# Optimization experiments

Measured on AMD Instinct MI355X. Metric: run time of the kernel, lower is better.

## Reference

```python
import jax, jax.numpy as jnp
import numpy as np
from jax import lax

B, C, N, T, K = 16, 64, 512, 64, 3
EPS = 1e-5


def _bn(x, g, b):
    # training-mode BatchNorm2d over (B, H=N, W=T) per channel
    m = jnp.mean(x, axis=(0, 2, 3), keepdims=True)
    v = jnp.var(x, axis=(0, 2, 3), keepdims=True)
    return (x - m) * lax.rsqrt(v + EPS) * g[None, :, None, None] + b[None, :, None, None]


def _conv(x, w, b, pad):
    y = lax.conv_general_dilated(x, w, (1, 1), ((0, 0), pad),
                                 dimension_numbers=('NCHW', 'OIHW', 'NCHW'))
    return y + b[None, :, None, None]


def setup_inputs() -> dict:
    key = jax.random.key(0)
    ks = jax.random.split(key, 8)
    xav = lambda k, sh, fi, fo: jax.random.normal(k, sh, jnp.float32) * np.sqrt(2.0 / (fi + fo))
    return {
        'x': jax.random.normal(ks[0], (B, C, N, T), jnp.float32),
        'adj_mx': jax.random.normal(ks[1], (K, N, N), jnp.float32) / np.sqrt(N),
        'cheb_w': xav(ks[2], (K, C, C), C, C),
        'cheb_b': jnp.zeros((C,), jnp.float32),
        'w1': xav(ks[3], (C, C, 1, 3), 3 * C, 3 * C),
        'b1': jnp.zeros((C,), jnp.float32),
        'g1': jnp.ones((C,), jnp.float32),
        'be1': jnp.zeros((C,), jnp.float32),
        'w2': xav(ks[4], (C, C, 1, 3), 3 * C, 3 * C),
        'b2': jnp.zeros((C,), jnp.float32),
        'g2': jnp.ones((C,), jnp.float32),
        'be2': jnp.zeros((C,), jnp.float32),
        'gate_w': xav(ks[5], (C, 2 * C, 1, 1), 2 * C, C),
        'gate_b': jnp.zeros((C,), jnp.float32),
        'res_w': xav(ks[6], (C, C, 1, 1), C, C),
        'res_b': jnp.zeros((C,), jnp.float32),
        'g3': jnp.ones((C,), jnp.float32),
        'be3': jnp.zeros((C,), jnp.float32),
    }


def _forward(x, adj_mx, cheb_w, cheb_b, w1, b1, g1, be1, w2, b2, g2, be2,
             gate_w, gate_b, res_w, res_b, g3, be3):
    # ChebFilterBlock: out[b,o,n,t] = sum_{k,i,m} x[b,i,m,t] adj[k,m,n] W[k,i,o] + bias
    spatial = jnp.einsum('bimt,kmn,kio->bont', x, adj_mx, cheb_w) \
              + cheb_b[None, :, None, None]
    # temporal branch: two (1,3) convs with BN+ReLU
    t = jax.nn.relu(_bn(_conv(x, w1, b1, (1, 1)), g1, be1))
    t = jax.nn.relu(_bn(_conv(t, w2, b2, (1, 1)), g2, be2))
    # gated fusion
    comb = jnp.concatenate([spatial, t], axis=1)
    gate = jax.nn.sigmoid(_conv(comb, gate_w, gate_b, (0, 0)))
    res = _conv(x, res_w, res_b, (0, 0))
    out = gate * spatial + (1.0 - gate) * t + res
    return _bn(out, g3, be3)


def reference(x, adj_mx, cheb_w, cheb_b, w1, b1, g1, be1, w2, b2, g2, be2,
              gate_w, gate_b, res_w, res_b, g3, be3):
    return _forward(x, adj_mx, cheb_w, cheb_b, w1, b1, g1, be1, w2, b2, g2, be2,
                    gate_w, gate_b, res_w, res_b, g3, be3)
```

## Files before the change

kernel.cpp:

```cpp
#include <hip/hip_runtime.h>
#include <hip/hip_bf16.h>
#include <cstdint>

#define BB 16
#define CC 64
#define NN 512
#define TT 64
#define KCH 3
#define PP (BB*NN*TT)
#define EPSB 1e-5f

typedef __bf16 bf16;
typedef __bf16 bf16x8 __attribute__((ext_vector_type(8)));
typedef __bf16 bf16x4 __attribute__((ext_vector_type(4)));
typedef float  f32x4  __attribute__((ext_vector_type(4)));

#define MFMA16(A,Bv,Cv) __builtin_amdgcn_mfma_f32_16x16x32_bf16((A),(Bv),(Cv),0,0,0)

__device__ __forceinline__ void gload_lds16(const bf16* g, bf16* l){
  __builtin_amdgcn_global_load_lds(
      (const __attribute__((address_space(1))) void*)g,
      (__attribute__((address_space(3))) void*)l, 16, 0, 0);
}

__global__ __launch_bounds__(256) void k_adjT(const float* __restrict__ adj,
                                              bf16* __restrict__ adjb){
  int idx = blockIdx.x*256 + threadIdx.x;
  int m = idx & 511, n = (idx >> 9) & 511, k = idx >> 18;
  adjb[idx] = (bf16)adj[((size_t)(k*512 + m))*512 + n];
}

__global__ __launch_bounds__(256) void k_wprep(const float* __restrict__ w1,
    const float* __restrict__ w2, const float* __restrict__ cw,
    const float* __restrict__ gw, const float* __restrict__ rw,
    bf16* __restrict__ w1p, bf16* __restrict__ w2p, bf16* __restrict__ cp,
    bf16* __restrict__ gp, bf16* __restrict__ rp){
  int tid = threadIdx.x;
  for (int e = tid; e < 6*2048; e += 256){
    int j = e&7, lane = (e>>3)&63, cf = (e>>9)&3, ks = e>>11;
    int k = ks*32 + (lane>>4)*8 + j, col = cf*16 + (lane&15);
    int kk = k >> 6, i = k & 63;
    w1p[e] = (bf16)w1[(col*64 + i)*3 + kk];
    w2p[e] = (bf16)w2[(col*64 + i)*3 + kk];
    cp[e]  = (bf16)cw[((size_t)kk*64 + i)*64 + col];
  }
  for (int e = tid; e < 4*2048; e += 256){
    int j = e&7, lane = (e>>3)&63, cf = (e>>9)&3, ks = e>>11;
    int k = ks*32 + (lane>>4)*8 + j, col = cf*16 + (lane&15);
    gp[e] = (bf16)gw[col*128 + k];
  }
  for (int e = tid; e < 2*2048; e += 256){
    int j = e&7, lane = (e>>3)&63, cf = (e>>9)&3, ks = e>>11;
    int k = ks*32 + (lane>>4)*8 + j, col = cf*16 + (lane&15);
    rp[e] = (bf16)rw[col*64 + k];
  }
}

__global__ __launch_bounds__(256) void k_xlb(const float* __restrict__ x,
                                             bf16* __restrict__ xlb){
  __shared__ float tile[64][65];
  int bn = blockIdx.x; int b = bn >> 9, n = bn & 511;
  int tid = threadIdx.x;
  const float* xp = x + ((size_t)(b*64)*512 + n)*64;
  for (int p = 0; p < 4; ++p){
    int q = p*256 + tid;
    int i = q >> 4, tc = (q & 15)*4;
    float4 v = *reinterpret_cast<const float4*>(xp + (size_t)i*512*64 + tc);
    tile[i][tc+0] = v.x; tile[i][tc+1] = v.y; tile[i][tc+2] = v.z; tile[i][tc+3] = v.w;
  }
  __syncthreads();
  bf16* op = xlb + (size_t)bn*4096;
  for (int p = 0; p < 2; ++p){
    int v8 = p*256 + tid;
    int t = v8 >> 3, ic = (v8 & 7)*8;
    bf16x8 o;
    #pragma unroll
    for (int e = 0; e < 8; ++e) o[e] = (bf16)tile[ic+e][t];
    *reinterpret_cast<bf16x8*>(op + t*64 + ic) = o;
  }
}

__global__ __launch_bounds__(256) void k_xmt(const float* __restrict__ x,
                                             bf16* __restrict__ xmt){
  __shared__ bf16 T[32768];
  int bid = blockIdx.x;
  int b = bid >> 6, i0 = ((bid >> 3) & 7)*8, m0 = (bid & 7)*64;
  int tid = threadIdx.x;
  #pragma unroll 4
  for (int it = 0; it < 32; ++it){
    int flat = it*256 + tid;
    int t4 = flat & 15, m = (flat >> 4) & 63, i = flat >> 10;
    float4 v = *reinterpret_cast<const float4*>(
        x + ((size_t)((b*64 + i0 + i)*512) + (m0 + m))*64 + t4*4);
    int im = i*64 + m;
    int slot = t4 ^ ((m ^ i) & 15);
    bf16x4 pk; pk[0] = (bf16)v.x; pk[1] = (bf16)v.y; pk[2] = (bf16)v.z; pk[3] = (bf16)v.w;
    *reinterpret_cast<bf16x4*>(&T[im*64 + slot*4]) = pk;
  }
  __syncthreads();
  #pragma unroll 4
  for (int it = 0; it < 16; ++it){
    int flat = it*256 + tid;
    int mc = flat & 7, i = (flat >> 3) & 7, t = flat >> 6;
    bf16x8 o;
    #pragma unroll
    for (int e = 0; e < 8; ++e){
      int m = mc*8 + e;
      int slot = (t >> 2) ^ ((m ^ i) & 15);
      o[e] = T[(i*64 + m)*64 + slot*4 + (t & 3)];
    }
    *reinterpret_cast<bf16x8*>(
        &xmt[((size_t)((b*64 + t)*64) + i0 + i)*512 + m0 + mc*8]) = o;
  }
}

__global__ __launch_bounds__(256,4) void k_conv(const bf16* __restrict__ in,
    const bf16* __restrict__ wp, bf16* __restrict__ outp, float* __restrict__ part,
    const float* __restrict__ sc, const float* __restrict__ sh){
  int tid = threadIdx.x, w = tid >> 6, l = tid & 63, l15 = l & 15, lg = l >> 4;
  int blk = blockIdx.x;
  size_t rowbase = (size_t)blk * 64;
  const bf16* xr = in + rowbase * 64;
  int t = w*16 + l15;
  f32x4 acc[4] = {};
  #pragma unroll
  for (int ks = 0; ks < 6; ++ks){
    int dt = ks >> 1, kh = ks & 1;
    int ts = t + dt - 1;
    bf16x8 a = {};
    if (ts >= 0 && ts < 64){
      a = *reinterpret_cast<const bf16x8*>(xr + ts*64 + kh*32 + lg*8);
      if (sc){
        int i0 = kh*32 + lg*8;
        #pragma unroll
        for (int e = 0; e < 8; ++e){
          float f = (float)a[e]*sc[i0+e] + sh[i0+e];
          a[e] = (bf16)fmaxf(f, 0.f);
        }
      }
    }
    #pragma unroll
    for (int cf = 0; cf < 4; ++cf){
      bf16x8 bfr = *reinterpret_cast<const bf16x8*>(wp + ((ks*4 + cf)*64 + l)*8);
      acc[cf] = MFMA16(a, bfr, acc[cf]);
    }
  }
  __shared__ float ssum[4][4][16], ssq[4][4][16];
  #pragma unroll
  for (int cf = 0; cf < 4; ++cf){
    int o = cf*16 + l15;
    float s = 0.f, q = 0.f;
    #pragma unroll
    for (int r = 0; r < 4; ++r){
      float vv = acc[cf][r];
      int to = w*16 + lg*4 + r;
      outp[(rowbase + to)*64 + o] = (bf16)vv;
      s += vv; q += vv*vv;
    }
    s += __shfl_xor(s, 16); s += __shfl_xor(s, 32);
    q += __shfl_xor(q, 16); q += __shfl_xor(q, 32);
    if (lg == 0){ ssum[w][cf][l15] = s; ssq[w][cf][l15] = q; }
  }
  __syncthreads();
  if (tid < 64){
    int cf = tid >> 4, c = tid & 15;
    float s = ssum[0][cf][c]+ssum[1][cf][c]+ssum[2][cf][c]+ssum[3][cf][c];
    float q = ssq[0][cf][c]+ssq[1][cf][c]+ssq[2][cf][c]+ssq[3][cf][c];
    part[(size_t)blk*128 + tid*2]     = s;
    part[(size_t)blk*128 + tid*2 + 1] = q;
  }
}

__global__ __launch_bounds__(256) void k_stats(const float* __restrict__ part, int nb,
    const float* __restrict__ g, const float* __restrict__ be,
    float* __restrict__ sc, float* __restrict__ sh){
  int c = blockIdx.x, tid = threadIdx.x;
  float s = 0.f, q = 0.f;
  for (int i = tid; i < nb; i += 256){
    s += part[(size_t)i*128 + c*2];
    q += part[(size_t)i*128 + c*2 + 1];
  }
  __shared__ float rs[256], rq[256];
  rs[tid] = s; rq[tid] = q; __syncthreads();
  for (int st = 128; st > 0; st >>= 1){
    if (tid < st){ rs[tid] += rs[tid+st]; rq[tid] += rq[tid+st]; }
    __syncthreads();
  }
  if (tid == 0){
    float cnt = (float)PP;
    float mean = rs[0]/cnt, var = rq[0]/cnt - mean*mean;
    float r = rsqrtf(var + EPSB);
    sc[c] = g[c]*r;
    sh[c] = be[c] - mean*g[c]*r;
  }
}

__global__ __launch_bounds__(256,3) void k_gemm1(const bf16* __restrict__ xmt,
    const bf16* __restrict__ adjb, const bf16* __restrict__ cp,
    const float* __restrict__ cb, bf16* __restrict__ spm){
  __shared__ bf16 As[2][4096];
  __shared__ bf16 Bs[2][4096];
  __shared__ bf16 VT[64*128];

  int tid = threadIdx.x, w = tid >> 6, l = tid & 63, l15 = l & 15, lg = l >> 4;
  int wr = w >> 1, wc = w & 1;

  int orig = blockIdx.x;
  int wg = (orig & 7) * 256 + (orig >> 3);
  int jt = wg >> 2, nt = wg & 3;
  int J0 = jt*128, N0 = nt*128;

  const bf16* aglob = xmt + (size_t)J0*512;
  const bf16* bbase = adjb + (size_t)N0*512;

  auto stage = [&](int t){
    int buf = t & 1;
    const bf16* bg = bbase + (size_t)(t >> 4)*512*512;
    int m0 = (t & 15)*32;
    #pragma unroll
    for (int p = 0; p < 2; ++p){
      int idx = p*256 + tid;
      int r = idx >> 2, c = idx & 3;
      int cg = c ^ (r & 3);
      gload_lds16(aglob + (size_t)r*512 + m0 + cg*8,
                  &As[buf][(p*256 + w*64)*8]);
      gload_lds16(bg + (size_t)r*512 + m0 + cg*8,
                  &Bs[buf][(p*256 + w*64)*8]);
    }
  };

  f32x4 acc[4][4] = {};
  f32x4 acc2[4][4] = {};

  stage(0);
  for (int t = 0; t < 48; ++t){
    if (t < 47){
      stage(t+1);
      asm volatile("s_waitcnt vmcnt(4)" ::: "memory");
    } else {
      asm volatile("s_waitcnt vmcnt(0)" ::: "memory");
    }
    __builtin_amdgcn_s_barrier();
    __builtin_amdgcn_sched_barrier(0);

    int buf = t & 1;
    bf16x8 a[4], bb[4];
    #pragma unroll
    for (int rf = 0; rf < 4; ++rf){
      int row = wr*64 + rf*16 + l15;
      a[rf] = *reinterpret_cast<const bf16x8*>(
          &As[buf][row*32 + ((lg ^ (row & 3))*8)]);
    }
    #pragma unroll
    for (int cf = 0; cf < 4; ++cf){
      int row = wc*64 + cf*16 + l15;
      bb[cf] = *reinterpret_cast<const bf16x8*>(
          &Bs[buf][row*32 + ((lg ^ (row & 3))*8)]);
    }
    #pragma unroll
    for (int rf = 0; rf < 4; ++rf)
      #pragma unroll
      for (int cf = 0; cf < 4; ++cf)
        acc[rf][cf] = MFMA16(a[rf], bb[cf], acc[rf][cf]);

    asm volatile("s_waitcnt lgkmcnt(0)" ::: "memory");
    __builtin_amdgcn_sched_barrier(0);
    __builtin_amdgcn_s_barrier();

    if ((t & 15) == 15){
      int kk = t >> 4;
      #pragma unroll
      for (int h = 0; h < 2; ++h){
        if (wc == h){
          #pragma unroll
          for (int rf = 0; rf < 4; ++rf){
            int jb = wr*8 + rf*2 + (lg >> 1);
            #pragma unroll
            for (int cf = 0; cf < 4; ++cf){
              int nh = cf*16 + l15;
              bf16x4 pk;
              #pragma unroll
              for (int r = 0; r < 4; ++r) pk[r] = (bf16)acc[rf][cf][r];
              *reinterpret_cast<bf16x4*>(
                  &VT[nh*128 + ((jb ^ (nh & 15)) << 3) + ((lg & 1) << 2)]) = pk;
            }
          }
        }
        asm volatile("s_waitcnt lgkmcnt(0)" ::: "memory");
        __builtin_amdgcn_sched_barrier(0);
        __builtin_amdgcn_s_barrier();

        #pragma unroll
        for (int ks2 = 0; ks2 < 2; ++ks2){
          bf16x8 bc[4];
          #pragma unroll
          for (int cf = 0; cf < 4; ++cf)
            bc[cf] = *reinterpret_cast<const bf16x8*>(
                cp + (((kk*2 + ks2)*4 + cf)*64 + l)*8);
          #pragma unroll
          for (int rf2 = 0; rf2 < 2; ++rf2){
            int nh = (w & 1)*32 + rf2*16 + l15;
            int jb = (w >> 1)*8 + ks2*4 + lg;
            bf16x8 a2 = *reinterpret_cast<const bf16x8*>(
                &VT[nh*128 + ((jb ^ (nh & 15)) << 3)]);
            #pragma unroll
            for (int cf = 0; cf < 4; ++cf)
              acc2[h*2 + rf2][cf] = MFMA16(a2, bc[cf], acc2[h*2 + rf2][cf]);
          }
        }
        asm volatile("s_waitcnt lgkmcnt(0)" ::: "memory");
        __builtin_amdgcn_sched_barrier(0);
        __builtin_amdgcn_s_barrier();
      }
      #pragma unroll
      for (int rf = 0; rf < 4; ++rf)
        #pragma unroll
        for (int cf = 0; cf < 4; ++cf)
          acc[rf][cf] = (f32x4){0.f, 0.f, 0.f, 0.f};
    }
  }

  bf16* SP = VT;
  float cbv[4];
  #pragma unroll
  for (int cf = 0; cf < 4; ++cf) cbv[cf] = cb[cf*16 + l15];
  int b = jt >> 5, t0 = (jt & 31)*2;
  #pragma unroll
  for (int hr = 0; hr < 2; ++hr){
    if ((w >> 1) == hr){
      #pragma unroll
      for (int f = 0; f < 4; ++f){
        int h = f >> 1, rf2 = f & 1;
        int rowb = h*64 + (w & 1)*32 + rf2*16 + lg*4;
        #pragma unroll
        for (int cf = 0; cf < 4; ++cf){
          int o = cf*16 + l15;
          #pragma unroll
          for (int r = 0; r < 4; ++r)
            SP[(rowb + r)*64 + o] = (bf16)(acc2[f][cf][r] + cbv[cf]);
        }
      }
    }
    __syncthreads();
    #pragma unroll
    for (int q = 0; q < 4; ++q){
      int flat = q*256 + tid;
      int n = flat >> 3, oc = (flat & 7)*8;
      bf16x8 vv = *reinterpret_cast<const bf16x8*>(&SP[n*64 + oc]);
      *reinterpret_cast<bf16x8*>(
          &spm[(((size_t)b*512 + N0 + n)*64 + (t0 + hr))*64 + oc]) = vv;
    }
    __syncthreads();
  }
}

__global__ __launch_bounds__(256,4) void k_fusion(const bf16* __restrict__ spm,
    const bf16* __restrict__ t2, const bf16* __restrict__ xlb,
    const bf16* __restrict__ gp, const bf16* __restrict__ rp,
    const float* __restrict__ sc2, const float* __restrict__ sh2,
    const float* __restrict__ gateb, bf16* __restrict__ pre,
    float* __restrict__ part){
  int tid = threadIdx.x, w = tid >> 6, l = tid & 63, l15 = l & 15, lg = l >> 4;
  int blk = blockIdx.x;
  int b = blk >> 9, n = blk & 511;
  size_t rowbase = (size_t)blk * 64;
  int t = w*16 + l15;
  f32x4 ag[4] = {}, ar[4] = {};
  #pragma unroll
  for (int ks = 0; ks < 4; ++ks){
    bf16x8 a;
    if (ks < 2){
      a = *reinterpret_cast<const bf16x8*>(spm + (rowbase + t)*64 + ks*32 + lg*8);
    } else {
      int i0 = (ks-2)*32 + lg*8;
      bf16x8 raw = *reinterpret_cast<const bf16x8*>(t2 + (rowbase + t)*64 + i0);
      #pragma unroll
      for (int e = 0; e < 8; ++e){
        float f = (float)raw[e]*sc2[i0+e] + sh2[i0+e];
        a[e] = (bf16)fmaxf(f, 0.f);
      }
    }
    #pragma unroll
    for (int cf = 0; cf < 4; ++cf){
      bf16x8 bfr = *reinterpret_cast<const bf16x8*>(gp + ((ks*4 + cf)*64 + l)*8);
      ag[cf] = MFMA16(a, bfr, ag[cf]);
    }
  }
  #pragma unroll
  for (int ks = 0; ks < 2; ++ks){
    bf16x8 a = *reinterpret_cast<const bf16x8*>(xlb + (rowbase + t)*64 + ks*32 + lg*8);
    #pragma unroll
    for (int cf = 0; cf < 4; ++cf){
      bf16x8 bfr = *reinterpret_cast<const bf16x8*>(rp + ((ks*4 + cf)*64 + l)*8);
      ar[cf] = MFMA16(a, bfr, ar[cf]);
    }
  }
  __shared__ float ssum[4][4][16], ssq[4][4][16];
  int tb = w*16 + lg*4;
  #pragma unroll
  for (int cf = 0; cf < 4; ++cf){
    int o = cf*16 + l15;
    float gb = gateb[o], sco = sc2[o], sho = sh2[o];
    float s = 0.f, q = 0.f;
    bf16x4 ov;
    #pragma unroll
    for (int r = 0; r < 4; ++r){
      size_t row = rowbase + tb + r;
      float z = ag[cf][r] + gb;
      float g = 1.f/(1.f + __expf(-z));
      float spv = (float)spm[row*64 + o];
      float tv  = (float)t2[row*64 + o];
      tv = fmaxf(tv*sco + sho, 0.f);
      float val = g*spv + (1.f - g)*tv + ar[cf][r];
      ov[r] = (bf16)val;
      s += val; q += val*val;
    }
    *reinterpret_cast<bf16x4*>(pre + (((size_t)b*64 + o)*512 + n)*64 + tb) = ov;
    s += __shfl_xor(s, 16); s += __shfl_xor(s, 32);
    q += __shfl_xor(q, 16); q += __shfl_xor(q, 32);
    if (lg == 0){ ssum[w][cf][l15] = s; ssq[w][cf][l15] = q; }
  }
  __syncthreads();
  if (tid < 64){
    int cf = tid >> 4, c = tid & 15;
    float s = ssum[0][cf][c]+ssum[1][cf][c]+ssum[2][cf][c]+ssum[3][cf][c];
    float q = ssq[0][cf][c]+ssq[1][cf][c]+ssq[2][cf][c]+ssq[3][cf][c];
    part[(size_t)blk*128 + tid*2]     = s;
    part[(size_t)blk*128 + tid*2 + 1] = q;
  }
}

__global__ __launch_bounds__(256) void k_bn3(const bf16* __restrict__ pre,
    float* __restrict__ out,
    const float* __restrict__ sc, const float* __restrict__ sh){
  size_t total8 = (size_t)BB*CC*NN*TT/8;
  for (size_t i8 = (size_t)blockIdx.x*256 + threadIdx.x; i8 < total8;
       i8 += (size_t)gridDim.x*256){
    bf16x8 v = reinterpret_cast<const bf16x8*>(pre)[i8];
    int o = (int)(i8 >> 12) & 63;
    float a = sc[o], bsh = sh[o];
    float4 r0, r1;
    r0.x = (float)v[0]*a + bsh; r0.y = (float)v[1]*a + bsh;
    r0.z = (float)v[2]*a + bsh; r0.w = (float)v[3]*a + bsh;
    r1.x = (float)v[4]*a + bsh; r1.y = (float)v[5]*a + bsh;
    r1.z = (float)v[6]*a + bsh; r1.w = (float)v[7]*a + bsh;
    reinterpret_cast<float4*>(out)[i8*2]     = r0;
    reinterpret_cast<float4*>(out)[i8*2 + 1] = r1;
  }
}

extern "C" void kernel_launch(void* const* d_in, const int* in_sizes, int n_in,
                              void* d_out, int out_size, void* d_ws, size_t ws_size,
                              hipStream_t stream){
  (void)in_sizes; (void)n_in; (void)out_size; (void)ws_size;
  const float* x   = (const float*)d_in[0];
  const float* adj = (const float*)d_in[1];
  const float* cw  = (const float*)d_in[2];
  const float* cb  = (const float*)d_in[3];
  const float* w1  = (const float*)d_in[4];
  const float* g1  = (const float*)d_in[6];
  const float* be1 = (const float*)d_in[7];
  const float* w2  = (const float*)d_in[8];
  const float* g2  = (const float*)d_in[10];
  const float* be2 = (const float*)d_in[11];
  const float* gw  = (const float*)d_in[12];
  const float* gb  = (const float*)d_in[13];
  const float* rw  = (const float*)d_in[14];
  const float* g3  = (const float*)d_in[16];
  const float* be3 = (const float*)d_in[17];
  float* out = (float*)d_out;

  char* ws = (char*)d_ws;
  size_t off = 0;
  auto alloc = [&](size_t bytes)->char*{
    char* p = ws + off; off += (bytes + 255) & ~(size_t)255; return p;
  };
  bf16* xlb  = (bf16*)alloc((size_t)PP*64*2);
  bf16* xmt  = (bf16*)alloc((size_t)PP*64*2);
  bf16* t1   = (bf16*)alloc((size_t)PP*64*2);
  bf16* t2   = (bf16*)alloc((size_t)PP*64*2);
  bf16* spm  = t1;
  bf16* pre  = xmt;
  bf16* adjb = (bf16*)alloc((size_t)KCH*512*512*2);
  bf16* w1p  = (bf16*)alloc(6*2048*2);
  bf16* w2p  = (bf16*)alloc(6*2048*2);
  bf16* cp   = (bf16*)alloc(6*2048*2);
  bf16* gp   = (bf16*)alloc(4*2048*2);
  bf16* rp   = (bf16*)alloc(2*2048*2);
  float* part = (float*)alloc((size_t)8192*128*4);
  float* s1sc = (float*)alloc(256); float* s1sh = (float*)alloc(256);
  float* s2sc = (float*)alloc(256); float* s2sh = (float*)alloc(256);
  float* s3sc = (float*)alloc(256); float* s3sh = (float*)alloc(256);

  k_adjT <<<dim3(3072), dim3(256), 0, stream>>>(adj, adjb);
  k_wprep<<<dim3(1),    dim3(256), 0, stream>>>(w1, w2, cw, gw, rw, w1p, w2p, cp, gp, rp);
  k_xlb  <<<dim3(8192), dim3(256), 0, stream>>>(x, xlb);
  k_xmt  <<<dim3(1024), dim3(256), 0, stream>>>(x, xmt);

  k_conv <<<dim3(8192), dim3(256), 0, stream>>>(xlb, w1p, t1, part, nullptr, nullptr);
  k_stats<<<dim3(64),   dim3(256), 0, stream>>>(part, 8192, g1, be1, s1sc, s1sh);
  k_conv <<<dim3(8192), dim3(256), 0, stream>>>(t1, w2p, t2, part, s1sc, s1sh);
  k_stats<<<dim3(64),   dim3(256), 0, stream>>>(part, 8192, g2, be2, s2sc, s2sh);

  k_gemm1<<<dim3(2048), dim3(256), 0, stream>>>(xmt, adjb, cp, cb, spm);

  k_fusion<<<dim3(8192), dim3(256), 0, stream>>>(spm, t2, xlb, gp, rp,
                                                 s2sc, s2sh, gb, pre, part);
  k_stats<<<dim3(64),   dim3(256), 0, stream>>>(part, 8192, g3, be3, s3sc, s3sh);
  k_bn3  <<<dim3(2048), dim3(256), 0, stream>>>(pre, out, s3sc, s3sh);
}
```

Measured before the change: 656.2 us.

## Double k_gemm1 workgroup to 512 threads with 2x4 wave grid and new LDS swizzle

Rewrites the k_gemm1 work split from 4 waves to 8 waves per 128x128 tile. Each wave now holds half the accumulators, so register pressure drops and more waves can be resident on a CU. The global-to-LDS staging becomes one load per thread, and a second XOR term is added to the LDS swizzle to reduce bank conflicts. Tile offsets are precomputed outside the loop. The cost is more barrier participants and less MFMA work per wave between syncs.

```diff
diff --git a/kernel.cpp b/kernel.cpp
--- a/kernel.cpp
+++ b/kernel.cpp
@@ -195,7 +195,7 @@
   }
 }
 
-__global__ __launch_bounds__(256,3) void k_gemm1(const bf16* __restrict__ xmt,
+__global__ __launch_bounds__(512,4) void k_gemm1(const bf16* __restrict__ xmt,
     const bf16* __restrict__ adjb, const bf16* __restrict__ cp,
     const float* __restrict__ cb, bf16* __restrict__ spm){
   __shared__ bf16 As[2][4096];
@@ -203,7 +203,7 @@
   __shared__ bf16 VT[64*128];
 
   int tid = threadIdx.x, w = tid >> 6, l = tid & 63, l15 = l & 15, lg = l >> 4;
-  int wr = w >> 1, wc = w & 1;
+  int wr = w >> 2, wc = w & 3;
 
   int orig = blockIdx.x;
   int wg = (orig & 7) * 256 + (orig >> 3);
@@ -213,30 +213,38 @@
   const bf16* aglob = xmt + (size_t)J0*512;
   const bf16* bbase = adjb + (size_t)N0*512;
 
+  int sr = tid >> 2, sc = tid & 3;
+  int scg = sc ^ (sr & 3) ^ ((sr >> 2) & 3);
+  size_t soff = (size_t)sr*512 + scg*8;
+
   auto stage = [&](int t){
     int buf = t & 1;
-    const bf16* bg = bbase + (size_t)(t >> 4)*512*512;
+    const bf16* bg = bbase + (size_t)(t >> 4)*(512*512);
     int m0 = (t & 15)*32;
-    #pragma unroll
-    for (int p = 0; p < 2; ++p){
-      int idx = p*256 + tid;
-      int r = idx >> 2, c = idx & 3;
-      int cg = c ^ (r & 3);
-      gload_lds16(aglob + (size_t)r*512 + m0 + cg*8,
-                  &As[buf][(p*256 + w*64)*8]);
-      gload_lds16(bg + (size_t)r*512 + m0 + cg*8,
-                  &Bs[buf][(p*256 + w*64)*8]);
-    }
+    gload_lds16(aglob + soff + m0, &As[buf][tid*8]);
+    gload_lds16(bg    + soff + m0, &Bs[buf][tid*8]);
   };
 
-  f32x4 acc[4][4] = {};
-  f32x4 acc2[4][4] = {};
+  int aoff[4], boff[2];
+  #pragma unroll
+  for (int rf = 0; rf < 4; ++rf){
+    int row = wr*64 + rf*16 + l15;
+    aoff[rf] = row*32 + ((lg ^ (row & 3) ^ ((row >> 2) & 3))*8);
+  }
+  #pragma unroll
+  for (int cf = 0; cf < 2; ++cf){
+    int row = wc*32 + cf*16 + l15;
+    boff[cf] = row*32 + ((lg ^ (row & 3) ^ ((row >> 2) & 3))*8);
+  }
+
+  f32x4 acc[4][2] = {};
+  f32x4 acc2[2][4] = {};
 
   stage(0);
   for (int t = 0; t < 48; ++t){
     if (t < 47){
       stage(t+1);
-      asm volatile("s_waitcnt vmcnt(4)" ::: "memory");
+      asm volatile("s_waitcnt vmcnt(2)" ::: "memory");
     } else {
       asm volatile("s_waitcnt vmcnt(0)" ::: "memory");
     }
@@ -244,23 +252,17 @@
     __builtin_amdgcn_sched_barrier(0);
 
     int buf = t & 1;
-    bf16x8 a[4], bb[4];
-    #pragma unroll
-    for (int rf = 0; rf < 4; ++rf){
-      int row = wr*64 + rf*16 + l15;
-      a[rf] = *reinterpret_cast<const bf16x8*>(
-          &As[buf][row*32 + ((lg ^ (row & 3))*8)]);
-    }
-    #pragma unroll
-    for (int cf = 0; cf < 4; ++cf){
-      int row = wc*64 + cf*16 + l15;
-      bb[cf] = *reinterpret_cast<const bf16x8*>(
-          &Bs[buf][row*32 + ((lg ^ (row & 3))*8)]);
-    }
+    bf16x8 a[4], bb[2];
+    #pragma unroll
+    for (int rf = 0; rf < 4; ++rf)
+      a[rf] = *reinterpret_cast<const bf16x8*>(&As[buf][aoff[rf]]);
+    #pragma unroll
+    for (int cf = 0; cf < 2; ++cf)
+      bb[cf] = *reinterpret_cast<const bf16x8*>(&Bs[buf][boff[cf]]);
     #pragma unroll
     for (int rf = 0; rf < 4; ++rf)
       #pragma unroll
-      for (int cf = 0; cf < 4; ++cf)
+      for (int cf = 0; cf < 2; ++cf)
         acc[rf][cf] = MFMA16(a[rf], bb[cf], acc[rf][cf]);
 
     asm volatile("s_waitcnt lgkmcnt(0)" ::: "memory");
@@ -271,13 +273,13 @@
       int kk = t >> 4;
       #pragma unroll
       for (int h = 0; h < 2; ++h){
-        if (wc == h){
+        if ((wc >> 1) == h){
           #pragma unroll
           for (int rf = 0; rf < 4; ++rf){
             int jb = wr*8 + rf*2 + (lg >> 1);
             #pragma unroll
-            for (int cf = 0; cf < 4; ++cf){
-              int nh = cf*16 + l15;
+            for (int cf = 0; cf < 2; ++cf){
+              int nh = (wc & 1)*32 + cf*16 + l15;
               bf16x4 pk;
               #pragma unroll
               for (int r = 0; r < 4; ++r) pk[r] = (bf16)acc[rf][cf][r];
@@ -297,16 +299,13 @@
           for (int cf = 0; cf < 4; ++cf)
             bc[cf] = *reinterpret_cast<const bf16x8*>(
                 cp + (((kk*2 + ks2)*4 + cf)*64 + l)*8);
+          int nh = (w & 3)*16 + l15;
+          int jb = (w >> 2)*8 + ks2*4 + lg;
+          bf16x8 a2 = *reinterpret_cast<const bf16x8*>(
+              &VT[nh*128 + ((jb ^ (nh & 15)) << 3)]);
           #pragma unroll
-          for (int rf2 = 0; rf2 < 2; ++rf2){
-            int nh = (w & 1)*32 + rf2*16 + l15;
-            int jb = (w >> 1)*8 + ks2*4 + lg;
-            bf16x8 a2 = *reinterpret_cast<const bf16x8*>(
-                &VT[nh*128 + ((jb ^ (nh & 15)) << 3)]);
-            #pragma unroll
-            for (int cf = 0; cf < 4; ++cf)
-              acc2[h*2 + rf2][cf] = MFMA16(a2, bc[cf], acc2[h*2 + rf2][cf]);
-          }
+          for (int cf = 0; cf < 4; ++cf)
+            acc2[h][cf] = MFMA16(a2, bc[cf], acc2[h][cf]);
         }
         asm volatile("s_waitcnt lgkmcnt(0)" ::: "memory");
         __builtin_amdgcn_sched_barrier(0);
@@ -315,7 +314,7 @@
       #pragma unroll
       for (int rf = 0; rf < 4; ++rf)
         #pragma unroll
-        for (int cf = 0; cf < 4; ++cf)
+        for (int cf = 0; cf < 2; ++cf)
           acc[rf][cf] = (f32x4){0.f, 0.f, 0.f, 0.f};
     }
   }
@@ -327,24 +326,23 @@
   int b = jt >> 5, t0 = (jt & 31)*2;
   #pragma unroll
   for (int hr = 0; hr < 2; ++hr){
-    if ((w >> 1) == hr){
+    if ((w >> 2) == hr){
       #pragma unroll
-      for (int f = 0; f < 4; ++f){
-        int h = f >> 1, rf2 = f & 1;
-        int rowb = h*64 + (w & 1)*32 + rf2*16 + lg*4;
+      for (int h = 0; h < 2; ++h){
+        int rowb = h*64 + (w & 3)*16 + lg*4;
         #pragma unroll
         for (int cf = 0; cf < 4; ++cf){
           int o = cf*16 + l15;
           #pragma unroll
           for (int r = 0; r < 4; ++r)
-            SP[(rowb + r)*64 + o] = (bf16)(acc2[f][cf][r] + cbv[cf]);
+            SP[(rowb + r)*64 + o] = (bf16)(acc2[h][cf][r] + cbv[cf]);
         }
       }
     }
     __syncthreads();
     #pragma unroll
-    for (int q = 0; q < 4; ++q){
-      int flat = q*256 + tid;
+    for (int q = 0; q < 2; ++q){
+      int flat = q*512 + tid;
       int n = flat >> 3, oc = (flat & 7)*8;
       bf16x8 vv = *reinterpret_cast<const bf16x8*>(&SP[n*64 + oc]);
       *reinterpret_cast<bf16x8*>(
@@ -502,7 +500,7 @@
   k_conv <<<dim3(8192), dim3(256), 0, stream>>>(t1, w2p, t2, part, s1sc, s1sh);
   k_stats<<<dim3(64),   dim3(256), 0, stream>>>(part, 8192, g2, be2, s2sc, s2sh);
 
-  k_gemm1<<<dim3(2048), dim3(256), 0, stream>>>(xmt, adjb, cp, cb, spm);
+  k_gemm1<<<dim3(2048), dim3(512), 0, stream>>>(xmt, adjb, cp, cb, spm);
 
   k_fusion<<<dim3(8192), dim3(256), 0, stream>>>(spm, t2, xlb, gp, rp,
                                                  s2sc, s2sh, gb, pre, part);
```

Measured after the change: 609.2 us. 1.08x faster.
